# Performance work log

Measured on AMD Instinct MI355X. Metric: run time of the kernel, lower is better.

Reference implementation:

```python
import jax, jax.numpy as jnp
import numpy as np

N_NODES = 100000
AVG_DEG = 16
D_IN, D_HID, D_OUT = 128, 128, 64


def setup_inputs() -> dict:
    key = jax.random.key(0)
    k_x, k_w1, k_w2 = jax.random.split(key, 3)
    rng = np.random.default_rng(0)
    # random adjacency edges + self-loops (I + A)
    src = rng.integers(0, N_NODES, N_NODES * AVG_DEG)
    dst = rng.integers(0, N_NODES, N_NODES * AVG_DEG)
    loops = np.arange(N_NODES)
    src = np.concatenate([src, loops]).astype(np.int32)
    dst = np.concatenate([dst, loops]).astype(np.int32)
    # symmetric normalization D^{-1/2} (I+A) D^{-1/2}; deg = row sums of I+A
    deg = np.bincount(src, minlength=N_NODES).astype(np.float32)
    val = (1.0 / np.sqrt(deg[src] * deg[dst])).astype(np.float32)
    return {
        "x": jax.random.normal(k_x, (N_NODES, D_IN), dtype=jnp.float32),
        "W1": jax.random.normal(k_w1, (D_IN, D_HID), dtype=jnp.float32),
        "W2": jax.random.normal(k_w2, (D_HID, D_OUT), dtype=jnp.float32),
        "edge_src": jnp.asarray(src),
        "edge_dst": jnp.asarray(dst),
        "edge_val": jnp.asarray(val),
    }


def _gcn_layer(x, W, src, dst, val, n):
    xw = x @ W                               # dense GEMM: [N, d_out]
    msg = val[:, None] * xw[dst]             # gather along edges: [E, d_out]
    return jax.ops.segment_sum(msg, src, num_segments=n)  # A_hat @ (XW)


def reference(x, W1, W2, edge_src, edge_dst, edge_val):
    n = x.shape[0]
    h = jax.nn.relu(_gcn_layer(x, W1, edge_src, edge_dst, edge_val, n))
    h = jax.nn.relu(_gcn_layer(h, W2, edge_src, edge_dst, edge_val, n))
    return jax.nn.softmax(h, axis=-1)
```

## Files before the change

### kernel.cpp

```cpp
#include <hip/hip_runtime.h>
#include <hip/hip_fp16.h>
#include <math.h>

#define DHID 128
#define DOUT 64
#define EPB 4096
#define BUCK_SH 8

typedef _Float16 half8 __attribute__((ext_vector_type(8)));
typedef float f32x4 __attribute__((ext_vector_type(4)));

static inline size_t align_up(size_t v, size_t a) { return (v + a - 1) / a * a; }


__global__ __launch_bounds__(256) void k_bincount(const int* __restrict__ src, int* __restrict__ dir,
                                                  int* __restrict__ btot, int E, int nbuck, int nblka) {
    __shared__ int hist[512];
    int tid = threadIdx.x;
    for (int i = tid; i < nbuck; i += 256) hist[i] = 0;
    __syncthreads();
    int e0 = blockIdx.x * EPB;
    #pragma unroll
    for (int j = 0; j < EPB / 256; ++j) {
        int e = e0 + tid + j * 256;
        if (e < E) atomicAdd(&hist[src[e] >> BUCK_SH], 1);
    }
    __syncthreads();
    for (int i = tid; i < nbuck; i += 256) {
        int c = hist[i];
        dir[i * nblka + blockIdx.x] = c;
        if (c) atomicAdd(&btot[i], c);
    }
}

__global__ __launch_bounds__(256) void k_dirscan(int* __restrict__ dir, const int* __restrict__ btot,
                                                 int* __restrict__ bucketbase, int* __restrict__ off,
                                                 int n, int nbuck, int nblka, int E) {
    __shared__ int h[512], s4[128], redb[256];
    int tid = threadIdx.x, b = blockIdx.x;
    int s = 0;
    for (int i = tid; i < b; i += 256) s += btot[i];
    redb[tid] = s; __syncthreads();
    #pragma unroll
    for (int d = 128; d > 0; d >>= 1) {
        if (tid < d) redb[tid] += redb[tid + d];
        __syncthreads();
    }
    int base = redb[0];
    if (tid == 0) {
        bucketbase[b] = base;
        if (b == 0) off[n] = E;
        if (b == nbuck - 1) bucketbase[nbuck] = E;
    }
    for (int j = tid; j < nblka; j += 256) h[j] = dir[b * nblka + j];
    __syncthreads();
    int nq = (nblka + 3) >> 2;
    if (tid < nq) {
        int t = 0;
        #pragma unroll
        for (int j = 0; j < 4; ++j) { int idx = tid * 4 + j; if (idx < nblka) t += h[idx]; }
        s4[tid] = t;
    }
    __syncthreads();
    if (tid == 0) { int run = 0; for (int i = 0; i < nq; ++i) { int t = s4[i]; s4[i] = run; run += t; } }
    __syncthreads();
    if (tid < nq) {
        int run = s4[tid] + base;
        #pragma unroll
        for (int j = 0; j < 4; ++j) {
            int idx = tid * 4 + j;
            if (idx < nblka) { int t = h[idx]; dir[b * nblka + idx] = run; run += t; }
        }
    }
}

__global__ __launch_bounds__(256) void k_binwrite(const int* __restrict__ src, const int* __restrict__ dst,
                                                  const float* __restrict__ val, const int* __restrict__ dir,
                                                  int2* __restrict__ ctmp, int E, int nbuck, int nblka) {
    __shared__ int cur[512];
    int tid = threadIdx.x, blk = blockIdx.x;
    for (int i = tid; i < nbuck; i += 256) cur[i] = dir[i * nblka + blk];
    __syncthreads();
    int e0 = blk * EPB;
    #pragma unroll
    for (int j = 0; j < EPB / 256; ++j) {
        int e = e0 + tid + j * 256;
        if (e < E) {
            int s = src[e];
            int bk = s >> BUCK_SH;
            int p = atomicAdd(&cur[bk], 1);
            ctmp[p] = make_int2(((s & 255) << 17) | dst[e], __float_as_int(val[e]));
        }
    }
}

__global__ __launch_bounds__(256) void k_csrify(const int* __restrict__ bucketbase,
                                                const int2* __restrict__ ctmp, int2* __restrict__ cpair,
                                                int* __restrict__ off, int n) {
    __shared__ int h[256], loff[256], cur[256], s4[64];
    int tid = threadIdx.x, b = blockIdx.x;
    int base = bucketbase[b];
    int cnt = bucketbase[b + 1] - base;
    h[tid] = 0;
    __syncthreads();
    for (int i = tid; i < cnt; i += 256) atomicAdd(&h[ctmp[base + i].x >> 17], 1);
    __syncthreads();
    if (tid < 64) {
        int s = 0;
        #pragma unroll
        for (int j = 0; j < 4; ++j) s += h[tid * 4 + j];
        s4[tid] = s;
    }
    __syncthreads();
    if (tid == 0) { int run = 0; for (int i = 0; i < 64; ++i) { int t = s4[i]; s4[i] = run; run += t; } }
    __syncthreads();
    if (tid < 64) {
        int run = s4[tid];
        #pragma unroll
        for (int j = 0; j < 4; ++j) { int idx = tid * 4 + j; loff[idx] = run; run += h[idx]; }
    }
    __syncthreads();
    int node0 = b << BUCK_SH;
    int nodes_b = n - node0; if (nodes_b > 256) nodes_b = 256;
    if (tid < nodes_b) off[node0 + tid] = base + loff[tid];
    cur[tid] = loff[tid];
    __syncthreads();
    for (int i = tid; i < cnt; i += 256) {
        int2 v = ctmp[base + i];
        int sl = v.x >> 17;
        int p = atomicAdd(&cur[sl], 1);
        cpair[base + p] = make_int2(v.x & 0x1FFFF, v.y);
    }
}

__global__ __launch_bounds__(256) void k_wprep(const float* __restrict__ W1, const float* __restrict__ W2,
                                               _Float16* __restrict__ Wt1, _Float16* __restrict__ Wt2,
                                               int* __restrict__ btot, int nbuck) {
    int b = blockIdx.x, tid = threadIdx.x;
    int gid = b * 256 + tid;
    if (gid < nbuck) btot[gid] = 0;
    if (b < 64) {
        int m = b * 256 + tid;
        int c = m >> 7, k = m & 127;
        Wt1[m] = (_Float16)W1[(size_t)k * 128 + c];
    } else {
        int m = (b - 64) * 256 + tid;
        int c = m >> 7, k = m & 127;
        Wt2[m] = (_Float16)W2[(size_t)k * 64 + c];
    }
}

__global__ __launch_bounds__(256) void k_gemm1(const float* __restrict__ x, const _Float16* __restrict__ Wt1,
                                               __half* __restrict__ xw, int n) {
    __shared__ _Float16 Ws[128 * 128];
    int tid = threadIdx.x;
    int row0 = blockIdx.x * 64;

    #pragma unroll
    for (int m0 = 0; m0 < 2048; m0 += 256) {
        int m = tid + m0;
        int c = m >> 4, kq = m & 15;
        uint4 v = *(const uint4*)(Wt1 + (size_t)m * 8);
        int byte = (c * 256 + kq * 16) ^ ((c & 7) << 4);
        *(uint4*)((char*)Ws + byte) = v;
    }
    __syncthreads();

    int lane = tid & 63;
    int wid = tid >> 6;
    int rg = row0 + wid * 16 + (lane & 15); if (rg >= n) rg = n - 1;
    int kgrp = (lane >> 4) * 8;

    f32x4 acc[8];
    #pragma unroll
    for (int t = 0; t < 8; ++t) acc[t] = (f32x4){0.f, 0.f, 0.f, 0.f};

    #pragma unroll
    for (int kk = 0; kk < 128; kk += 32) {
        int ks = kk + kgrp;
        const float4* xp = (const float4*)(x + (size_t)rg * 128 + ks);
        float4 f0 = xp[0], f1 = xp[1];
        half8 a;
        a[0] = (_Float16)f0.x; a[1] = (_Float16)f0.y; a[2] = (_Float16)f0.z; a[3] = (_Float16)f0.w;
        a[4] = (_Float16)f1.x; a[5] = (_Float16)f1.y; a[6] = (_Float16)f1.z; a[7] = (_Float16)f1.w;
        #pragma unroll
        for (int t = 0; t < 8; ++t) {
            int c = t * 16 + (lane & 15);
            int bbyte = (c * 256 + ks * 2) ^ ((c & 7) << 4);
            half8 b = *(const half8*)((const char*)Ws + bbyte);
            acc[t] = __builtin_amdgcn_mfma_f32_16x16x32_f16(a, b, acc[t], 0, 0, 0);
        }
    }

    #pragma unroll
    for (int t = 0; t < 8; ++t) {
        int c = t * 16 + (lane & 15);
        #pragma unroll
        for (int j = 0; j < 4; ++j) {
            int rs = row0 + wid * 16 + (lane >> 4) * 4 + j;
            if (rs < n) xw[(size_t)rs * 128 + c] = __float2half(acc[t][j]);
        }
    }
}

__global__ __launch_bounds__(256) void k_gemm2(const __half* __restrict__ h1, const _Float16* __restrict__ Wt2,
                                               __half* __restrict__ hw, int n) {
    __shared__ _Float16 Ws[64 * 128];
    int tid = threadIdx.x;
    int row0 = blockIdx.x * 64;

    #pragma unroll
    for (int m0 = 0; m0 < 1024; m0 += 256) {
        int m = tid + m0;
        int c = m >> 4, kq = m & 15;
        uint4 v = *(const uint4*)(Wt2 + (size_t)m * 8);
        int byte = (c * 256 + kq * 16) ^ ((c & 7) << 4);
        *(uint4*)((char*)Ws + byte) = v;
    }
    __syncthreads();

    int lane = tid & 63;
    int wid = tid >> 6;
    int rg = row0 + wid * 16 + (lane & 15); if (rg >= n) rg = n - 1;
    int kgrp = (lane >> 4) * 8;

    f32x4 acc[4];
    #pragma unroll
    for (int t = 0; t < 4; ++t) acc[t] = (f32x4){0.f, 0.f, 0.f, 0.f};

    #pragma unroll
    for (int kk = 0; kk < 128; kk += 32) {
        int ks = kk + kgrp;
        half8 a = *(const half8*)((const void*)(h1 + (size_t)rg * 128 + ks));
        #pragma unroll
        for (int t = 0; t < 4; ++t) {
            int c = t * 16 + (lane & 15);
            int bbyte = (c * 256 + ks * 2) ^ ((c & 7) << 4);
            half8 b = *(const half8*)((const char*)Ws + bbyte);
            acc[t] = __builtin_amdgcn_mfma_f32_16x16x32_f16(a, b, acc[t], 0, 0, 0);
        }
    }

    #pragma unroll
    for (int t = 0; t < 4; ++t) {
        int c = t * 16 + (lane & 15);
        #pragma unroll
        for (int j = 0; j < 4; ++j) {
            int rs = row0 + wid * 16 + (lane >> 4) * 4 + j;
            if (rs < n) hw[(size_t)rs * 64 + c] = __float2half(acc[t][j]);
        }
    }
}

__global__ __launch_bounds__(256) void k_agg1(const __half* __restrict__ xw, const int* __restrict__ off,
                                              const int2* __restrict__ cpair,
                                              __half* __restrict__ h1, int n) {
    __shared__ int2 pbuf[4][64];
    int wave = threadIdx.x >> 6;
    int lane = threadIdx.x & 63;
    int node = blockIdx.x * 4 + wave;
    if (node >= n) return;
    int s = off[node], e = off[node + 1];
    float ax = 0.f, ay = 0.f;
    for (int c0 = s; c0 < e; c0 += 64) {
        int cnt = e - c0; if (cnt > 64) cnt = 64;
        if (lane < cnt) pbuf[wave][lane] = cpair[c0 + lane];
        int j = 0;
        for (; j + 8 <= cnt; j += 8) {
            int2 p[8];
            #pragma unroll
            for (int t = 0; t < 8; ++t) p[t] = pbuf[wave][j + t];
            float2 v[8];
            #pragma unroll
            for (int t = 0; t < 8; ++t)
                v[t] = __half22float2(((const __half2*)(xw + (size_t)p[t].x * 128))[lane]);
            #pragma unroll
            for (int t = 0; t < 8; ++t) {
                float w = __int_as_float(p[t].y);
                ax += w * v[t].x; ay += w * v[t].y;
            }
        }
        for (; j < cnt; ++j) {
            int2 p = pbuf[wave][j];
            float w = __int_as_float(p.y);
            float2 v = __half22float2(((const __half2*)(xw + (size_t)p.x * 128))[lane]);
            ax += w * v.x; ay += w * v.y;
        }
    }
    ((__half2*)(h1 + (size_t)node * 128))[lane] = __floats2half2_rn(fmaxf(ax, 0.f), fmaxf(ay, 0.f));
}

__global__ __launch_bounds__(256) void k_agg2(const __half* __restrict__ hw, const int* __restrict__ off,
                                              const int2* __restrict__ cpair,
                                              float* __restrict__ out, int n) {
    __shared__ int2 pbuf[4][64];
    int wave = threadIdx.x >> 6;
    int lane = threadIdx.x & 63;
    int node = blockIdx.x * 4 + wave;
    if (node >= n) return;
    int s = off[node], e = off[node + 1];
    float acc = 0.f;
    for (int c0 = s; c0 < e; c0 += 64) {
        int cnt = e - c0; if (cnt > 64) cnt = 64;
        if (lane < cnt) pbuf[wave][lane] = cpair[c0 + lane];
        int j = 0;
        for (; j + 8 <= cnt; j += 8) {
            int2 p[8];
            #pragma unroll
            for (int t = 0; t < 8; ++t) p[t] = pbuf[wave][j + t];
            float v[8];
            #pragma unroll
            for (int t = 0; t < 8; ++t)
                v[t] = __half2float(hw[(size_t)p[t].x * 64 + lane]);
            #pragma unroll
            for (int t = 0; t < 8; ++t)
                acc += __int_as_float(p[t].y) * v[t];
        }
        for (; j < cnt; ++j) {
            int2 p = pbuf[wave][j];
            acc += __int_as_float(p.y) * __half2float(hw[(size_t)p.x * 64 + lane]);
        }
    }
    acc = fmaxf(acc, 0.f);
    float m = acc;
    #pragma unroll
    for (int o = 32; o > 0; o >>= 1) m = fmaxf(m, __shfl_xor(m, o));
    float ex = expf(acc - m);
    float sum = ex;
    #pragma unroll
    for (int o = 32; o > 0; o >>= 1) sum += __shfl_xor(sum, o);
    out[(size_t)node * 64 + lane] = ex / sum;
}

extern "C" void kernel_launch(void* const* d_in, const int* in_sizes, int n_in,
                              void* d_out, int out_size, void* d_ws, size_t ws_size,
                              hipStream_t stream) {
    const float* x = (const float*)d_in[0];
    const float* W1 = (const float*)d_in[1];
    const float* W2 = (const float*)d_in[2];
    const int* esrc = (const int*)d_in[3];
    const int* edst = (const int*)d_in[4];
    const float* evalv = (const float*)d_in[5];
    int n = in_sizes[0] / DHID;
    int E = in_sizes[3];

    int nbuck = (n + 255) >> BUCK_SH;
    int nblka = (E + EPB - 1) / EPB;

    char* p = (char*)d_ws;
    int* off = (int*)p;        p += align_up((size_t)(n + 1) * 4, 256);
    int* bucketbase = (int*)p; p += align_up((size_t)(nbuck + 1) * 4, 256);
    int* btot = (int*)p;       p += align_up((size_t)nbuck * 4, 256);
    int* dir = (int*)p;        p += align_up((size_t)nbuck * nblka * 4, 256);
    int2* ctmp = (int2*)p;     p += align_up((size_t)E * 8, 256);
    int2* cpair = (int2*)p;    p += align_up((size_t)E * 8, 256);
    _Float16* Wt1 = (_Float16*)p; p += align_up((size_t)128 * 128 * 2, 256);
    _Float16* Wt2 = (_Float16*)p; p += align_up((size_t)64 * 128 * 2, 256);
    __half* xw = (__half*)p;   p += align_up((size_t)n * DHID * 2, 256);
    __half* h1 = (__half*)p;   p += align_up((size_t)n * DHID * 2, 256);
    __half* hw2 = xw;

    k_wprep<<<96, 256, 0, stream>>>(W1, W2, Wt1, Wt2, btot, nbuck);
    k_gemm1<<<(n + 63) / 64, 256, 0, stream>>>(x, Wt1, xw, n);
    k_bincount<<<nblka, 256, 0, stream>>>(esrc, dir, btot, E, nbuck, nblka);
    k_dirscan<<<nbuck, 256, 0, stream>>>(dir, btot, bucketbase, off, n, nbuck, nblka, E);
    k_binwrite<<<nblka, 256, 0, stream>>>(esrc, edst, evalv, dir, ctmp, E, nbuck, nblka);
    k_csrify<<<nbuck, 256, 0, stream>>>(bucketbase, ctmp, cpair, off, n);
    k_agg1<<<(n + 3) / 4, 256, 0, stream>>>(xw, off, cpair, h1, n);
    k_gemm2<<<(n + 63) / 64, 256, 0, stream>>>(h1, Wt2, hw2, n);
    k_agg2<<<(n + 3) / 4, 256, 0, stream>>>(hw2, off, cpair, (float*)d_out, n);
}
```

Measured before the change: 203.9 us.

## Merge prep kernels into heterogeneous launches and use nontemporal edge/output access

Combines the weight-transpose prep with the edge bincount into one launch, and the first GEMM with the bucket directory scan into another, using block-index ranges to pick the role. The btot array is now zeroed with a memset. This drops launch count and lets independent work share the GPU. Edge-pair loads in both aggregation kernels and the h1 and output stores become nontemporal, to keep streamed data from evicting the gathered feature rows in cache. The merged GEMM kernel reserves the 32KB weight tile of shared memory even for scan blocks, which may lower their occupancy.

```diff
diff --git a/kernel.cpp b/kernel.cpp
--- a/kernel.cpp
+++ b/kernel.cpp
@@ -12,64 +12,132 @@
 
 static inline size_t align_up(size_t v, size_t a) { return (v + a - 1) / a * a; }
 
-
-__global__ __launch_bounds__(256) void k_bincount(const int* __restrict__ src, int* __restrict__ dir,
-                                                  int* __restrict__ btot, int E, int nbuck, int nblka) {
+__global__ __launch_bounds__(256) void k_prep(const int* __restrict__ src, int* __restrict__ dir,
+                                              int* __restrict__ btot, int E, int nbuck, int nblka,
+                                              const float* __restrict__ W1, const float* __restrict__ W2,
+                                              _Float16* __restrict__ Wt1, _Float16* __restrict__ Wt2) {
     __shared__ int hist[512];
     int tid = threadIdx.x;
-    for (int i = tid; i < nbuck; i += 256) hist[i] = 0;
-    __syncthreads();
-    int e0 = blockIdx.x * EPB;
-    #pragma unroll
-    for (int j = 0; j < EPB / 256; ++j) {
-        int e = e0 + tid + j * 256;
-        if (e < E) atomicAdd(&hist[src[e] >> BUCK_SH], 1);
-    }
-    __syncthreads();
-    for (int i = tid; i < nbuck; i += 256) {
-        int c = hist[i];
-        dir[i * nblka + blockIdx.x] = c;
-        if (c) atomicAdd(&btot[i], c);
-    }
-}
-
-__global__ __launch_bounds__(256) void k_dirscan(int* __restrict__ dir, const int* __restrict__ btot,
-                                                 int* __restrict__ bucketbase, int* __restrict__ off,
-                                                 int n, int nbuck, int nblka, int E) {
+    int blk = blockIdx.x;
+    if (blk < nblka) {
+        for (int i = tid; i < nbuck; i += 256) hist[i] = 0;
+        __syncthreads();
+        int e0 = blk * EPB;
+        #pragma unroll
+        for (int j = 0; j < EPB / 256; ++j) {
+            int e = e0 + tid + j * 256;
+            if (e < E) atomicAdd(&hist[src[e] >> BUCK_SH], 1);
+        }
+        __syncthreads();
+        for (int i = tid; i < nbuck; i += 256) {
+            int c = hist[i];
+            dir[i * nblka + blk] = c;
+            if (c) atomicAdd(&btot[i], c);
+        }
+    } else {
+        int b = blk - nblka;
+        if (b < 64) {
+            int m = b * 256 + tid;
+            int c = m >> 7, k = m & 127;
+            Wt1[m] = (_Float16)W1[(size_t)k * 128 + c];
+        } else {
+            int m = (b - 64) * 256 + tid;
+            int c = m >> 7, k = m & 127;
+            Wt2[m] = (_Float16)W2[(size_t)k * 64 + c];
+        }
+    }
+}
+
+__global__ __launch_bounds__(256) void k_g1ds(const float* __restrict__ x, const _Float16* __restrict__ Wt1,
+                                              __half* __restrict__ xw, int n, int ng1,
+                                              int* __restrict__ dir, const int* __restrict__ btot,
+                                              int* __restrict__ bucketbase, int* __restrict__ off,
+                                              int nbuck, int nblka, int E) {
+    __shared__ _Float16 Ws[128 * 128];
     __shared__ int h[512], s4[128], redb[256];
-    int tid = threadIdx.x, b = blockIdx.x;
-    int s = 0;
-    for (int i = tid; i < b; i += 256) s += btot[i];
-    redb[tid] = s; __syncthreads();
-    #pragma unroll
-    for (int d = 128; d > 0; d >>= 1) {
-        if (tid < d) redb[tid] += redb[tid + d];
-        __syncthreads();
-    }
-    int base = redb[0];
-    if (tid == 0) {
-        bucketbase[b] = base;
-        if (b == 0) off[n] = E;
-        if (b == nbuck - 1) bucketbase[nbuck] = E;
-    }
-    for (int j = tid; j < nblka; j += 256) h[j] = dir[b * nblka + j];
-    __syncthreads();
-    int nq = (nblka + 3) >> 2;
-    if (tid < nq) {
-        int t = 0;
-        #pragma unroll
-        for (int j = 0; j < 4; ++j) { int idx = tid * 4 + j; if (idx < nblka) t += h[idx]; }
-        s4[tid] = t;
-    }
-    __syncthreads();
-    if (tid == 0) { int run = 0; for (int i = 0; i < nq; ++i) { int t = s4[i]; s4[i] = run; run += t; } }
-    __syncthreads();
-    if (tid < nq) {
-        int run = s4[tid] + base;
-        #pragma unroll
-        for (int j = 0; j < 4; ++j) {
-            int idx = tid * 4 + j;
-            if (idx < nblka) { int t = h[idx]; dir[b * nblka + idx] = run; run += t; }
+    int tid = threadIdx.x;
+    if (blockIdx.x < ng1) {
+        int row0 = blockIdx.x * 64;
+        #pragma unroll
+        for (int m0 = 0; m0 < 2048; m0 += 256) {
+            int m = tid + m0;
+            int c = m >> 4, kq = m & 15;
+            uint4 v = *(const uint4*)(Wt1 + (size_t)m * 8);
+            int byte = (c * 256 + kq * 16) ^ ((c & 7) << 4);
+            *(uint4*)((char*)Ws + byte) = v;
+        }
+        __syncthreads();
+
+        int lane = tid & 63;
+        int wid = tid >> 6;
+        int rg = row0 + wid * 16 + (lane & 15); if (rg >= n) rg = n - 1;
+        int kgrp = (lane >> 4) * 8;
+
+        f32x4 acc[8];
+        #pragma unroll
+        for (int t = 0; t < 8; ++t) acc[t] = (f32x4){0.f, 0.f, 0.f, 0.f};
+
+        #pragma unroll
+        for (int kk = 0; kk < 128; kk += 32) {
+            int ks = kk + kgrp;
+            const float4* xp = (const float4*)(x + (size_t)rg * 128 + ks);
+            float4 f0 = xp[0], f1 = xp[1];
+            half8 a;
+            a[0] = (_Float16)f0.x; a[1] = (_Float16)f0.y; a[2] = (_Float16)f0.z; a[3] = (_Float16)f0.w;
+            a[4] = (_Float16)f1.x; a[5] = (_Float16)f1.y; a[6] = (_Float16)f1.z; a[7] = (_Float16)f1.w;
+            #pragma unroll
+            for (int t = 0; t < 8; ++t) {
+                int c = t * 16 + (lane & 15);
+                int bbyte = (c * 256 + ks * 2) ^ ((c & 7) << 4);
+                half8 b = *(const half8*)((const char*)Ws + bbyte);
+                acc[t] = __builtin_amdgcn_mfma_f32_16x16x32_f16(a, b, acc[t], 0, 0, 0);
+            }
+        }
+
+        #pragma unroll
+        for (int t = 0; t < 8; ++t) {
+            int c = t * 16 + (lane & 15);
+            #pragma unroll
+            for (int j = 0; j < 4; ++j) {
+                int rs = row0 + wid * 16 + (lane >> 4) * 4 + j;
+                if (rs < n) xw[(size_t)rs * 128 + c] = __float2half(acc[t][j]);
+            }
+        }
+    } else {
+        int b = blockIdx.x - ng1;
+        int s = 0;
+        for (int i = tid; i < b; i += 256) s += btot[i];
+        redb[tid] = s; __syncthreads();
+        #pragma unroll
+        for (int d = 128; d > 0; d >>= 1) {
+            if (tid < d) redb[tid] += redb[tid + d];
+            __syncthreads();
+        }
+        int base = redb[0];
+        if (tid == 0) {
+            bucketbase[b] = base;
+            if (b == 0) off[n] = E;
+            if (b == nbuck - 1) bucketbase[nbuck] = E;
+        }
+        for (int j = tid; j < nblka; j += 256) h[j] = dir[b * nblka + j];
+        __syncthreads();
+        int nq = (nblka + 3) >> 2;
+        if (tid < nq) {
+            int t = 0;
+            #pragma unroll
+            for (int j = 0; j < 4; ++j) { int idx = tid * 4 + j; if (idx < nblka) t += h[idx]; }
+            s4[tid] = t;
+        }
+        __syncthreads();
+        if (tid == 0) { int run = 0; for (int i = 0; i < nq; ++i) { int t = s4[i]; s4[i] = run; run += t; } }
+        __syncthreads();
+        if (tid < nq) {
+            int run = s4[tid] + base;
+            #pragma unroll
+            for (int j = 0; j < 4; ++j) {
+                int idx = tid * 4 + j;
+                if (idx < nblka) { int t = h[idx]; dir[b * nblka + idx] = run; run += t; }
+            }
         }
     }
 }
@@ -130,76 +198,6 @@
         int sl = v.x >> 17;
         int p = atomicAdd(&cur[sl], 1);
         cpair[base + p] = make_int2(v.x & 0x1FFFF, v.y);
-    }
-}
-
-__global__ __launch_bounds__(256) void k_wprep(const float* __restrict__ W1, const float* __restrict__ W2,
-                                               _Float16* __restrict__ Wt1, _Float16* __restrict__ Wt2,
-                                               int* __restrict__ btot, int nbuck) {
-    int b = blockIdx.x, tid = threadIdx.x;
-    int gid = b * 256 + tid;
-    if (gid < nbuck) btot[gid] = 0;
-    if (b < 64) {
-        int m = b * 256 + tid;
-        int c = m >> 7, k = m & 127;
-        Wt1[m] = (_Float16)W1[(size_t)k * 128 + c];
-    } else {
-        int m = (b - 64) * 256 + tid;
-        int c = m >> 7, k = m & 127;
-        Wt2[m] = (_Float16)W2[(size_t)k * 64 + c];
-    }
-}
-
-__global__ __launch_bounds__(256) void k_gemm1(const float* __restrict__ x, const _Float16* __restrict__ Wt1,
-                                               __half* __restrict__ xw, int n) {
-    __shared__ _Float16 Ws[128 * 128];
-    int tid = threadIdx.x;
-    int row0 = blockIdx.x * 64;
-
-    #pragma unroll
-    for (int m0 = 0; m0 < 2048; m0 += 256) {
-        int m = tid + m0;
-        int c = m >> 4, kq = m & 15;
-        uint4 v = *(const uint4*)(Wt1 + (size_t)m * 8);
-        int byte = (c * 256 + kq * 16) ^ ((c & 7) << 4);
-        *(uint4*)((char*)Ws + byte) = v;
-    }
-    __syncthreads();
-
-    int lane = tid & 63;
-    int wid = tid >> 6;
-    int rg = row0 + wid * 16 + (lane & 15); if (rg >= n) rg = n - 1;
-    int kgrp = (lane >> 4) * 8;
-
-    f32x4 acc[8];
-    #pragma unroll
-    for (int t = 0; t < 8; ++t) acc[t] = (f32x4){0.f, 0.f, 0.f, 0.f};
-
-    #pragma unroll
-    for (int kk = 0; kk < 128; kk += 32) {
-        int ks = kk + kgrp;
-        const float4* xp = (const float4*)(x + (size_t)rg * 128 + ks);
-        float4 f0 = xp[0], f1 = xp[1];
-        half8 a;
-        a[0] = (_Float16)f0.x; a[1] = (_Float16)f0.y; a[2] = (_Float16)f0.z; a[3] = (_Float16)f0.w;
-        a[4] = (_Float16)f1.x; a[5] = (_Float16)f1.y; a[6] = (_Float16)f1.z; a[7] = (_Float16)f1.w;
-        #pragma unroll
-        for (int t = 0; t < 8; ++t) {
-            int c = t * 16 + (lane & 15);
-            int bbyte = (c * 256 + ks * 2) ^ ((c & 7) << 4);
-            half8 b = *(const half8*)((const char*)Ws + bbyte);
-            acc[t] = __builtin_amdgcn_mfma_f32_16x16x32_f16(a, b, acc[t], 0, 0, 0);
-        }
-    }
-
-    #pragma unroll
-    for (int t = 0; t < 8; ++t) {
-        int c = t * 16 + (lane & 15);
-        #pragma unroll
-        for (int j = 0; j < 4; ++j) {
-            int rs = row0 + wid * 16 + (lane >> 4) * 4 + j;
-            if (rs < n) xw[(size_t)rs * 128 + c] = __float2half(acc[t][j]);
-        }
     }
 }
 
@@ -264,7 +262,10 @@
     float ax = 0.f, ay = 0.f;
     for (int c0 = s; c0 < e; c0 += 64) {
         int cnt = e - c0; if (cnt > 64) cnt = 64;
-        if (lane < cnt) pbuf[wave][lane] = cpair[c0 + lane];
+        if (lane < cnt) {
+            long long pk = __builtin_nontemporal_load((const long long*)(cpair + c0 + lane));
+            pbuf[wave][lane] = make_int2((int)(pk & 0xFFFFFFFFLL), (int)(pk >> 32));
+        }
         int j = 0;
         for (; j + 8 <= cnt; j += 8) {
             int2 p[8];
@@ -287,7 +288,9 @@
             ax += w * v.x; ay += w * v.y;
         }
     }
-    ((__half2*)(h1 + (size_t)node * 128))[lane] = __floats2half2_rn(fmaxf(ax, 0.f), fmaxf(ay, 0.f));
+    __half2 hv = __floats2half2_rn(fmaxf(ax, 0.f), fmaxf(ay, 0.f));
+    unsigned u = *(unsigned*)&hv;
+    __builtin_nontemporal_store(u, (unsigned*)(h1 + (size_t)node * 128) + lane);
 }
 
 __global__ __launch_bounds__(256) void k_agg2(const __half* __restrict__ hw, const int* __restrict__ off,
@@ -302,7 +305,10 @@
     float acc = 0.f;
     for (int c0 = s; c0 < e; c0 += 64) {
         int cnt = e - c0; if (cnt > 64) cnt = 64;
-        if (lane < cnt) pbuf[wave][lane] = cpair[c0 + lane];
+        if (lane < cnt) {
+            long long pk = __builtin_nontemporal_load((const long long*)(cpair + c0 + lane));
+            pbuf[wave][lane] = make_int2((int)(pk & 0xFFFFFFFFLL), (int)(pk >> 32));
+        }
         int j = 0;
         for (; j + 8 <= cnt; j += 8) {
             int2 p[8];
@@ -329,7 +335,7 @@
     float sum = ex;
     #pragma unroll
     for (int o = 32; o > 0; o >>= 1) sum += __shfl_xor(sum, o);
-    out[(size_t)node * 64 + lane] = ex / sum;
+    __builtin_nontemporal_store(ex / sum, out + (size_t)node * 64 + lane);
 }
 
 extern "C" void kernel_launch(void* const* d_in, const int* in_sizes, int n_in,
@@ -346,6 +352,7 @@
 
     int nbuck = (n + 255) >> BUCK_SH;
     int nblka = (E + EPB - 1) / EPB;
+    int ng1 = (n + 63) / 64;
 
     char* p = (char*)d_ws;
     int* off = (int*)p;        p += align_up((size_t)(n + 1) * 4, 256);
@@ -360,10 +367,10 @@
     __half* h1 = (__half*)p;   p += align_up((size_t)n * DHID * 2, 256);
     __half* hw2 = xw;
 
-    k_wprep<<<96, 256, 0, stream>>>(W1, W2, Wt1, Wt2, btot, nbuck);
-    k_gemm1<<<(n + 63) / 64, 256, 0, stream>>>(x, Wt1, xw, n);
-    k_bincount<<<nblka, 256, 0, stream>>>(esrc, dir, btot, E, nbuck, nblka);
-    k_dirscan<<<nbuck, 256, 0, stream>>>(dir, btot, bucketbase, off, n, nbuck, nblka, E);
+    hipMemsetAsync(btot, 0, (size_t)nbuck * 4, stream);
+    k_prep<<<nblka + 96, 256, 0, stream>>>(esrc, dir, btot, E, nbuck, nblka, W1, W2, Wt1, Wt2);
+    k_g1ds<<<ng1 + nbuck, 256, 0, stream>>>(x, Wt1, xw, n, ng1, dir, btot, bucketbase, off,
+                                            nbuck, nblka, E);
     k_binwrite<<<nblka, 256, 0, stream>>>(esrc, edst, evalv, dir, ctmp, E, nbuck, nblka);
     k_csrify<<<nbuck, 256, 0, stream>>>(bucketbase, ctmp, cpair, off, n);
     k_agg1<<<(n + 3) / 4, 256, 0, stream>>>(xw, off, cpair, h1, n);
```

After: 211.2 us. +3.6%, slower.
